# Kernel tuning notes

Measured on AMD Instinct MI355X. Metric: run time of the kernel, lower is better.

The kernel has to match this reference:

```python
import jax, jax.numpy as jnp
import numpy as np

CUTOFFS = [0, 10000, 20000, 40000, 50000]  # cutoff_ends incl. 0 and n_token
D_PROJ = 1024
D_EMBED = 1024
DIV_VAL = 4
N_TOKENS = 4096  # len*bsz flattened


def setup_inputs() -> dict:
    key = jax.random.key(0)
    ks = jax.random.split(key, 12)
    scale = 0.02
    sizes = [CUTOFFS[i + 1] - CUTOFFS[i] for i in range(4)]
    dims = [D_EMBED // DIV_VAL ** i for i in range(4)]  # 1024, 256, 64, 16
    inp = {
        "hidden": jax.random.normal(ks[0], (N_TOKENS, D_PROJ), jnp.float32),
        "target": jax.random.randint(ks[1], (N_TOKENS,), 0, CUTOFFS[-1]),
    }
    for i in range(4):
        inp[f"w{i}"] = jax.random.normal(ks[2 + i], (sizes[i], dims[i]), jnp.float32) * scale
        inp[f"b{i}"] = jnp.zeros((sizes[i],), jnp.float32)  # bias_scale=0.0 -> zeros
        inp[f"p{i}"] = jax.random.normal(ks[6 + i], (D_PROJ, dims[i]), jnp.float32) * scale
    inp["cluster_weight"] = jax.random.normal(ks[10], (3, D_EMBED), jnp.float32) * scale
    inp["cluster_bias"] = jnp.zeros((3,), jnp.float32)
    return inp


def reference(hidden, target, w0, b0, p0, w1, b1, p1, w2, b2, p2, w3, b3, p3,
              cluster_weight, cluster_bias):
    # head = shortlist weights + cluster logits rows  -> [10003, d_embed]
    head_w = jnp.concatenate([w0, cluster_weight], axis=0)
    head_b = jnp.concatenate([b0, cluster_bias], axis=0)
    head_logit = (hidden @ p0) @ head_w.T + head_b          # [N, 10003]
    head_lp = jax.nn.log_softmax(head_logit, axis=-1)
    rows = jnp.arange(hidden.shape[0])
    head_size = head_w.shape[0]

    # cluster 0 (shortlist): gather head log-prob at target
    mask0 = target < CUTOFFS[1]
    lp = jnp.where(mask0, head_lp[rows, jnp.clip(target, 0, CUTOFFS[1] - 1)], 0.0)

    # tail clusters i=1..3: head_logprob[:, -i] + tail log-prob at (target - l_idx)
    for i, (w, b, p) in enumerate([(w1, b1, p1), (w2, b2, p2), (w3, b3, p3)], start=1):
        l, r = CUTOFFS[i], CUTOFFS[i + 1]
        mask = (target >= l) & (target < r)
        tail_lp = jax.nn.log_softmax((hidden @ p) @ w.T + b, axis=-1)  # [N, r-l]
        g = tail_lp[rows, jnp.clip(target - l, 0, r - l - 1)]
        lp = lp + jnp.where(mask, head_lp[:, head_size - i] + g, 0.0)

    return -lp.mean()
```

## Files before the change

kernel.cpp:

```cpp
#include <hip/hip_runtime.h>
#include <hip/hip_fp8.h>
#include <math.h>

typedef __bf16 bf16;
typedef __attribute__((ext_vector_type(8))) __bf16 bf16x8;
typedef __attribute__((ext_vector_type(4))) float f32x4;
typedef __attribute__((ext_vector_type(16))) float f32x16;
typedef __attribute__((ext_vector_type(8))) int i32x8;

#define M_TOK 4096
#define MREF 8.0f


__device__ __forceinline__ void gl_lds16(const void* g, void* l) {
  __builtin_amdgcn_global_load_lds(
      (const __attribute__((address_space(1))) unsigned int*)g,
      (__attribute__((address_space(3))) unsigned int*)l, 16, 0, 0);
}

__device__ __forceinline__ int xcd_swz(int idx, int nwg) {
  int xcd = idx & 7, pos = idx >> 3;
  int q = nwg >> 3, r = nwg & 7;
  int base = xcd < r ? xcd * (q + 1) : r * (q + 1) + (xcd - r) * q;
  return base + pos;
}

__device__ __forceinline__ unsigned char f2fp8(float v) {
  __hip_fp8_e4m3 h(v);
  return (unsigned char)h.__x;
}
__device__ __forceinline__ float fp82f(unsigned char b) {
  __hip_fp8_e4m3 h;
  h.__x = (__hip_fp8_storage_t)b;
  return (float)h;
}

struct bf16x4s { bf16 a, b, c, d; };


#define NB0 4096
#define NB1 10240
#define NB2 2528
#define NB3 1256
#define NB4 316
#define NB5 352
#define NB6 198

__global__ __launch_bounds__(256) void prep(
    const float* __restrict__ hidden, const float* __restrict__ w0,
    const float* __restrict__ cw, const float* __restrict__ w1,
    const float* __restrict__ w2, const float* __restrict__ w3,
    const float* __restrict__ p0, const float* __restrict__ p1,
    const float* __restrict__ p2, const float* __restrict__ p3,
    const float* __restrict__ b0, const float* __restrict__ cb,
    const float* __restrict__ b1, const float* __restrict__ b2,
    const float* __restrict__ b3, const int* __restrict__ target,
    unsigned char* __restrict__ hiddenF8, unsigned char* __restrict__ headwF8,
    bf16* __restrict__ w1p, bf16* __restrict__ w2p, bf16* __restrict__ w3p,
    unsigned char* __restrict__ pF8,
    float* __restrict__ headb, float* __restrict__ t1b,
    float* __restrict__ t2b, float* __restrict__ t3b,
    int* __restrict__ r1, int* __restrict__ r2, int* __restrict__ r3,
    int* __restrict__ posmap, int* __restrict__ counts) {
  __shared__ float tile[64][65];
  __shared__ unsigned long long sd[256];
  int b = blockIdx.x, t = threadIdx.x;
  if (b < NB0) {
    long i = (long)b * 256 + t;
    float4 v = ((const float4*)hidden)[i];
    unsigned int u = (unsigned int)f2fp8(v.x) | ((unsigned int)f2fp8(v.y) << 8) |
                     ((unsigned int)f2fp8(v.z) << 16) | ((unsigned int)f2fp8(v.w) << 24);
    ((unsigned int*)hiddenF8)[i] = u;
    return;
  }
  b -= NB0;
  if (b < NB1) {
    long i = (long)b * 256 + t;
    int row = (int)(i >> 8), c4 = ((int)i & 255) * 4;
    float4 v;
    if (row < 10000)      v = *(const float4*)(w0 + (long)row * 1024 + c4);
    else if (row < 10003) v = *(const float4*)(cw + (long)(row - 10000) * 1024 + c4);
    else                  v = make_float4(0.f, 0.f, 0.f, 0.f);
    unsigned int u = (unsigned int)f2fp8(v.x) | ((unsigned int)f2fp8(v.y) << 8) |
                     ((unsigned int)f2fp8(v.z) << 16) | ((unsigned int)f2fp8(v.w) << 24);
    ((unsigned int*)headwF8)[i] = u;
    return;
  }
  b -= NB1;
  if (b < NB2) {
    long i = (long)b * 256 + t;
    int row = (int)(i >> 6), c4 = ((int)i & 63) * 4;
    float4 v = row < 10000 ? *(const float4*)(w1 + (long)row * 256 + c4)
                           : make_float4(0.f, 0.f, 0.f, 0.f);
    bf16x4s o; o.a = (bf16)v.x; o.b = (bf16)v.y; o.c = (bf16)v.z; o.d = (bf16)v.w;
    ((bf16x4s*)w1p)[i] = o;
    return;
  }
  b -= NB2;
  if (b < NB3) {
    long i = (long)b * 256 + t;
    int row = (int)(i >> 4), c4 = ((int)i & 15) * 4;
    float4 v = row < 20000 ? *(const float4*)(w2 + (long)row * 64 + c4)
                           : make_float4(0.f, 0.f, 0.f, 0.f);
    bf16x4s o; o.a = (bf16)v.x; o.b = (bf16)v.y; o.c = (bf16)v.z; o.d = (bf16)v.w;
    ((bf16x4s*)w2p)[i] = o;
    return;
  }
  b -= NB3;
  if (b < NB4) {
    long i = (long)b * 256 + t;
    int row = (int)(i >> 3), c4 = ((int)i & 7) * 4;
    float4 v = (row < 10000 && c4 < 16) ? *(const float4*)(w3 + (long)row * 16 + c4)
                                        : make_float4(0.f, 0.f, 0.f, 0.f);
    bf16x4s o; o.a = (bf16)v.x; o.b = (bf16)v.y; o.c = (bf16)v.z; o.d = (bf16)v.w;
    ((bf16x4s*)w3p)[i] = o;
    return;
  }
  b -= NB4;
  if (b < NB5) {
    int tk = b & 15, tn = b >> 4;
    int kb = tk * 64, nb = tn * 64;
    const float* src; int N, segn;
    if (tn < 16)      { src = p0; N = 1024; segn = nb; }
    else if (tn < 20) { src = p1; N = 256;  segn = nb - 1024; }
    else if (tn < 21) { src = p2; N = 64;   segn = 0; }
    else              { src = p3; N = 16;   segn = 0; }
    int tx = t & 63, ty = t >> 6;
#pragma unroll
    for (int kk = ty; kk < 64; kk += 4)
      tile[kk][tx] = (segn + tx < N) ? src[(long)(kb + kk) * N + segn + tx] : 0.f;
    __syncthreads();
#pragma unroll
    for (int nn = ty; nn < 64; nn += 4)
      pF8[(long)(nb + nn) * 1024 + kb + tx] = f2fp8(tile[tx][nn]);
    return;
  }
  b -= NB5;
  if (b < NB6) {
    int i = b * 256 + t;
    if (i < 10240) {
      headb[i] = i < 10000 ? b0[i] : (i < 10003 ? cb[i - 10000] : -3.0e38f);
    } else if (i < 10240 + 10112) {
      int j = i - 10240; t1b[j] = j < 10000 ? b1[j] : -3.0e38f;
    } else if (i < 10240 + 10112 + 20096) {
      int j = i - 10240 - 10112; t2b[j] = j < 20000 ? b2[j] : -3.0e38f;
    } else if (i < 10240 + 10112 + 20096 + 10112) {
      int j = i - 10240 - 10112 - 20096; t3b[j] = j < 10000 ? b3[j] : -3.0e38f;
    }
    return;
  }
  {
    int c1 = 0, c2 = 0, c3 = 0;
#pragma unroll
    for (int j = 0; j < 16; ++j) {
      int tt = target[t * 16 + j];
      if (tt >= 10000) { if (tt < 20000) ++c1; else if (tt < 40000) ++c2; else ++c3; }
    }
    unsigned long long packed = (unsigned long long)c1 |
                                ((unsigned long long)c2 << 21) |
                                ((unsigned long long)c3 << 42);
    sd[t] = packed;
    __syncthreads();
    for (int off = 1; off < 256; off <<= 1) {
      unsigned long long add = t >= off ? sd[t - off] : 0ULL;
      __syncthreads();
      sd[t] += add;
      __syncthreads();
    }
    unsigned long long excl = sd[t] - packed;
    const unsigned long long M21 = (1ULL << 21) - 1;
    int p1i = (int)(excl & M21), p2i = (int)((excl >> 21) & M21), p3i = (int)(excl >> 42);
#pragma unroll
    for (int j = 0; j < 16; ++j) {
      int row = t * 16 + j;
      int tt = target[row];
      if (tt >= 10000) {
        if (tt < 20000)      { r1[p1i] = row; posmap[row] = p1i; ++p1i; }
        else if (tt < 40000) { r2[p2i] = row; posmap[row] = p2i; ++p2i; }
        else                 { r3[p3i] = row; posmap[row] = p3i; ++p3i; }
      }
    }
    if (t == 255) {
      unsigned long long tot = sd[255];
      counts[1] = (int)(tot & M21);
      counts[2] = (int)((tot >> 21) & M21);
      counts[3] = (int)(tot >> 42);
    }
  }
}


template<int MODE>
__global__ __launch_bounds__(256, 2) void f8gemm(
    const unsigned char* __restrict__ A,
    const unsigned char* __restrict__ B,
    unsigned char* __restrict__ Cf8, bf16* __restrict__ Cbf,
    const float* __restrict__ bias,
    float* __restrict__ Ps, int nslot) {
  int bid = blockIdx.x;
  int xcd = bid & 7, pos = bid >> 3;
  int tile = pos >> 2;
  int rowblk = (xcd << 2) | (pos & 3);
  int rowbase = rowblk * 128;
  int tid = threadIdx.x;
  int w = tid >> 6, l = tid & 63;
  int l31 = l & 31, lh = l >> 5;
  int wr = w >> 1, wc = w & 1;

  __shared__ __align__(16) unsigned char As[2][128 * 128];
  __shared__ __align__(16) unsigned char Bs[2][128 * 128];

  int srow = tid >> 3;
  int slot = tid & 7;
  const unsigned char* ga[4];
  const unsigned char* gb[4];
#pragma unroll
  for (int c = 0; c < 4; ++c) {
    int lrow = c * 32 + srow;
    int gslot = slot ^ ((lrow ^ (lrow >> 3)) & 7);
    ga[c] = A + (long)(rowbase + lrow) * 1024 + gslot * 16;
    gb[c] = B + (long)(tile * 128 + lrow) * 1024 + gslot * 16;
  }

  f32x16 acc[2][2];
#pragma unroll
  for (int m = 0; m < 2; ++m)
#pragma unroll
    for (int n = 0; n < 2; ++n)
#pragma unroll
      for (int g = 0; g < 16; ++g) acc[m][n][g] = 0.f;

#pragma unroll
  for (int c = 0; c < 4; ++c) {
    gl_lds16(ga[c], &As[0][c * 4096 + tid * 16]);
    gl_lds16(gb[c], &Bs[0][c * 4096 + tid * 16]);
  }

  int cur = 0;
#pragma unroll
  for (int i = 0; i < 8; ++i) {
    if (i < 7) {
      int nxt = cur ^ 1;
      int k0 = (i + 1) * 128;
#pragma unroll
      for (int c = 0; c < 4; ++c) {
        gl_lds16(ga[c] + k0, &As[nxt][c * 4096 + tid * 16]);
        gl_lds16(gb[c] + k0, &Bs[nxt][c * 4096 + tid * 16]);
      }
      asm volatile("s_waitcnt vmcnt(8)" ::: "memory");
    } else {
      asm volatile("s_waitcnt vmcnt(0)" ::: "memory");
    }
    __builtin_amdgcn_s_barrier();
    __builtin_amdgcn_sched_barrier(0);

    const unsigned char* Ab = &As[cur][0];
    const unsigned char* Bb = &Bs[cur][0];
#pragma unroll
    for (int kk = 0; kk < 2; ++kk) {
      i32x8 af[2], bfr[2];
#pragma unroll
      for (int m = 0; m < 2; ++m) {
        int ar = wr * 64 + m * 32 + l31;
        int f = (ar ^ (ar >> 3)) & 7;
        int s0 = (kk * 4 + lh * 2) ^ f;
        int s1 = (kk * 4 + lh * 2 + 1) ^ f;
        int4 lo = *(const int4*)(Ab + ar * 128 + s0 * 16);
        int4 hi = *(const int4*)(Ab + ar * 128 + s1 * 16);
        af[m][0] = lo.x; af[m][1] = lo.y; af[m][2] = lo.z; af[m][3] = lo.w;
        af[m][4] = hi.x; af[m][5] = hi.y; af[m][6] = hi.z; af[m][7] = hi.w;
      }
#pragma unroll
      for (int n = 0; n < 2; ++n) {
        int br = wc * 64 + n * 32 + l31;
        int f = (br ^ (br >> 3)) & 7;
        int s0 = (kk * 4 + lh * 2) ^ f;
        int s1 = (kk * 4 + lh * 2 + 1) ^ f;
        int4 lo = *(const int4*)(Bb + br * 128 + s0 * 16);
        int4 hi = *(const int4*)(Bb + br * 128 + s1 * 16);
        bfr[n][0] = lo.x; bfr[n][1] = lo.y; bfr[n][2] = lo.z; bfr[n][3] = lo.w;
        bfr[n][4] = hi.x; bfr[n][5] = hi.y; bfr[n][6] = hi.z; bfr[n][7] = hi.w;
      }
#pragma unroll
      for (int m = 0; m < 2; ++m)
#pragma unroll
        for (int n = 0; n < 2; ++n)
          acc[m][n] = __builtin_amdgcn_mfma_scale_f32_32x32x64_f8f6f4(
              af[m], bfr[n], acc[m][n], 0, 0, 0, 0x7F7F7F7F, 0, 0x7F7F7F7F);
    }
    __builtin_amdgcn_s_barrier();
    cur ^= 1;
  }
  __builtin_amdgcn_sched_barrier(0);

  if (MODE == 0) {
    unsigned char* Ls = &As[0][0];
    int col0 = tile * 128;
    if (col0 < 1024) {
#pragma unroll
      for (int m = 0; m < 2; ++m)
#pragma unroll
        for (int n = 0; n < 2; ++n) {
          int col = wc * 64 + n * 32 + l31;
#pragma unroll
          for (int g = 0; g < 16; ++g) {
            int row = wr * 64 + m * 32 + (g & 3) + 8 * (g >> 2) + 4 * lh;
            Ls[row * 128 + col] = f2fp8(acc[m][n][g]);
          }
        }
      __syncthreads();
      int row = tid >> 1, half = tid & 1;
      unsigned char* gp = Cf8 + (long)(rowbase + row) * 1024 + col0 + half * 64;
#pragma unroll
      for (int j = 0; j < 4; ++j)
        *(int4*)(gp + j * 16) = *(const int4*)(Ls + tid * 64 + j * 16);
    } else {
      bf16* Lb = (bf16*)Ls;
#pragma unroll
      for (int m = 0; m < 2; ++m)
#pragma unroll
        for (int n = 0; n < 2; ++n) {
          int col = wc * 64 + n * 32 + l31;
#pragma unroll
          for (int g = 0; g < 16; ++g) {
            int row = wr * 64 + m * 32 + (g & 3) + 8 * (g >> 2) + 4 * lh;
            Lb[row * 128 + col] = (bf16)acc[m][n][g];
          }
        }
      __syncthreads();
      int row = tid >> 1, half = tid & 1;
      bf16* gp = Cbf + (long)(rowbase + row) * 384 + (col0 - 1024) + half * 64;
#pragma unroll
      for (int j = 0; j < 8; ++j)
        *(int4*)(gp + j * 8) = *(const int4*)(Ls + tid * 128 + j * 16);
    }
  } else {
    float rs[2][16];
#pragma unroll
    for (int m = 0; m < 2; ++m)
#pragma unroll
      for (int g = 0; g < 16; ++g) rs[m][g] = 0.f;
    int col0 = tile * 128;
#pragma unroll
    for (int n = 0; n < 2; ++n) {
      float bv = bias[col0 + wc * 64 + n * 32 + l31];
#pragma unroll
      for (int m = 0; m < 2; ++m)
#pragma unroll
        for (int g = 0; g < 16; ++g)
          rs[m][g] += __expf(acc[m][n][g] + bv - MREF);
    }
#pragma unroll
    for (int m = 0; m < 2; ++m)
#pragma unroll
      for (int g = 0; g < 16; ++g) {
        float v = rs[m][g];
        v += __shfl_xor(v, 1);
        v += __shfl_xor(v, 2);
        v += __shfl_xor(v, 4);
        v += __shfl_xor(v, 8);
        v += __shfl_xor(v, 16);
        rs[m][g] = v;
      }
    if (l31 == 0) {
      int slotP = tile * 2 + wc;
#pragma unroll
      for (int m = 0; m < 2; ++m)
#pragma unroll
        for (int g = 0; g < 16; ++g) {
          int row = rowbase + wr * 64 + m * 32 + (g & 3) + 8 * (g >> 2) + 4 * lh;
          Ps[(long)row * nslot + slotP] = rs[m][g];
        }
    }
  }
}


template<int K>
__global__ __launch_bounds__(256, 3) void tail_lse(
    const bf16* __restrict__ A, int lda,
    const bf16* __restrict__ B, int nTiles, int tpb,
    const float* __restrict__ bias,
    float* __restrict__ Ps, int nslot,
    const int* __restrict__ rowidx, const int* __restrict__ counts, int cluster) {
  int wg = xcd_swz(blockIdx.x, gridDim.x);
  int split = wg >> 5;
  int rowblk = wg & 31;
  int rowbase = rowblk * 128;
  int nc = counts[cluster];
  if (rowbase >= nc) return;
  int tid = threadIdx.x;
  int w = tid >> 6, llo = tid & 15, lhi = (tid >> 4) & 3;
  int wr = w >> 1, wc = w & 1;

  __shared__ __align__(16) bf16 As[128 * 32];
  __shared__ __align__(16) bf16 Bs[128 * 32];

  int srow = tid >> 2;
  int selem = (tid & 3) * 8;
  int sr0 = rowbase + srow, sr1 = sr0 + 64;
  sr0 = rowidx[sr0 < nc ? sr0 : nc - 1];
  sr1 = rowidx[sr1 < nc ? sr1 : nc - 1];
  const bf16* ga0 = A + (long)sr0 * lda + selem;
  const bf16* ga1 = A + (long)sr1 * lda + selem;
  bf16* la0 = As + tid * 8;
  bf16* la1 = As + 2048 + tid * 8;
  bf16* lb0 = Bs + tid * 8;
  bf16* lb1 = Bs + 2048 + tid * 8;

  float rs[4][4];
#pragma unroll
  for (int a = 0; a < 4; ++a)
#pragma unroll
    for (int bq = 0; bq < 4; ++bq) rs[a][bq] = 0.f;

  int t0 = split * tpb;
  int tE = t0 + tpb; if (tE > nTiles) tE = nTiles;

  for (int tile = t0; tile < tE; ++tile) {
    int col0 = tile * 128;
    const bf16* gb0 = B + (long)(col0 + srow) * K + selem;
    const bf16* gb1 = gb0 + (long)64 * K;

    f32x4 acc[4][4];
    f32x4 zero = {0.f, 0.f, 0.f, 0.f};
#pragma unroll
    for (int a = 0; a < 4; ++a)
#pragma unroll
      for (int bq = 0; bq < 4; ++bq) acc[a][bq] = zero;

    for (int k0 = 0; k0 < K; k0 += 32) {
      gl_lds16(ga0 + k0, la0);
      gl_lds16(ga1 + k0, la1);
      gl_lds16(gb0 + k0, lb0);
      gl_lds16(gb1 + k0, lb1);
      __syncthreads();
      bf16x8 af[4], bf_[4];
#pragma unroll
      for (int m = 0; m < 4; ++m)
        af[m] = *(const bf16x8*)(As + (wr * 64 + m * 16 + llo) * 32 + lhi * 8);
#pragma unroll
      for (int n = 0; n < 4; ++n)
        bf_[n] = *(const bf16x8*)(Bs + (wc * 64 + n * 16 + llo) * 32 + lhi * 8);
#pragma unroll
      for (int m = 0; m < 4; ++m)
#pragma unroll
        for (int n = 0; n < 4; ++n)
          acc[m][n] = __builtin_amdgcn_mfma_f32_16x16x32_bf16(af[m], bf_[n], acc[m][n], 0, 0, 0);
      __syncthreads();
    }

    float bv[4];
#pragma unroll
    for (int n = 0; n < 4; ++n) bv[n] = bias[col0 + wc * 64 + n * 16 + llo];
#pragma unroll
    for (int mm = 0; mm < 4; ++mm)
#pragma unroll
      for (int r = 0; r < 4; ++r)
#pragma unroll
        for (int n = 0; n < 4; ++n)
          rs[mm][r] += __expf(acc[mm][n][r] + bv[n] - MREF);
  }

#pragma unroll
  for (int mm = 0; mm < 4; ++mm) {
#pragma unroll
    for (int r = 0; r < 4; ++r) {
      float vv = rs[mm][r];
      vv += __shfl_xor(vv, 1);
      vv += __shfl_xor(vv, 2);
      vv += __shfl_xor(vv, 4);
      vv += __shfl_xor(vv, 8);
      if (llo == 0) {
        int crow = rowbase + wr * 64 + mm * 16 + lhi * 4 + r;
        Ps[(long)crow * nslot + (split * 2 + wc)] = vv;
      }
    }
  }
}


__global__ __launch_bounds__(256) void merge_lp(
    const int* __restrict__ target, const int* __restrict__ posmap,
    const unsigned char* __restrict__ projF8, const unsigned char* __restrict__ headw,
    const float* __restrict__ headb, const bf16* __restrict__ projT,
    const bf16* __restrict__ w1p, const float* __restrict__ t1b,
    const bf16* __restrict__ w2p, const float* __restrict__ t2b,
    const bf16* __restrict__ w3p, const float* __restrict__ t3b,
    const float* __restrict__ hs, int NSH,
    const float* __restrict__ s1, int NS1,
    const float* __restrict__ s2, int NS2,
    const float* __restrict__ s3, int NS3,
    float* __restrict__ lp) {
  int lane = threadIdx.x & 63;
  int row = (blockIdx.x * 256 + threadIdx.x) >> 6;
  if (row >= M_TOK) return;

  float sh = 0.f;
  for (int sp = lane; sp < NSH; sp += 64) sh += hs[(long)row * NSH + sp];
#pragma unroll
  for (int off = 1; off < 64; off <<= 1) sh += __shfl_xor(sh, off);
  float lseh = MREF + __logf(sh);

  float a[16];
  const unsigned char* ap = projF8 + (long)row * 1024 + lane * 16;
#pragma unroll
  for (int j = 0; j < 16; ++j) a[j] = fp82f(ap[j]);
  int t = target[row];
  int c0 = t < 10000 ? t : 9999;
  float hd[4];
#pragma unroll
  for (int q = 0; q < 4; ++q) {
    int col = q == 0 ? c0 : 9999 + q;
    const unsigned char* wp = headw + (long)col * 1024 + lane * 16;
    float d = 0.f;
#pragma unroll
    for (int j = 0; j < 16; ++j) d += a[j] * fp82f(wp[j]);
#pragma unroll
    for (int off = 1; off < 64; off <<= 1) d += __shfl_xor(d, off);
    hd[q] = d + headb[col];
  }

  float res;
  if (t < 10000) {
    res = hd[0] - lseh;
  } else {
    const float* sP; const bf16* wP; const float* bP;
    int NS, q, Kt, offT, base;
    if (t < 20000)      { sP = s1; wP = w1p; bP = t1b; NS = NS1; q = 3; Kt = 256; offT = 0;   base = 10000; }
    else if (t < 40000) { sP = s2; wP = w2p; bP = t2b; NS = NS2; q = 2; Kt = 64;  offT = 256; base = 20000; }
    else                { sP = s3; wP = w3p; bP = t3b; NS = NS3; q = 1; Kt = 32;  offT = 320; base = 40000; }
    int pos = posmap[row];
    float ss = 0.f;
    for (int sp = lane; sp < NS; sp += 64) ss += sP[(long)pos * NS + sp];
#pragma unroll
    for (int off = 1; off < 64; off <<= 1) ss += __shfl_xor(ss, off);
    float lset = MREF + __logf(ss);
    int wrow = t - base;
    float gt = 0.f;
    for (int k = lane; k < Kt; k += 64)
      gt += (float)projT[(long)row * 384 + offT + k] * (float)wP[(long)wrow * Kt + k];
#pragma unroll
    for (int off = 1; off < 64; off <<= 1) gt += __shfl_xor(gt, off);
    gt += bP[wrow];
    res = (hd[q] - lseh) + (gt - lset);
  }
  if (lane == 0) lp[row] = res;
}

__global__ void neg_mean(const float* __restrict__ lp, float* __restrict__ out) {
  __shared__ float red[256];
  float s = 0.f;
  for (int i = threadIdx.x; i < M_TOK; i += 256) s += lp[i];
  red[threadIdx.x] = s;
  __syncthreads();
  for (int o = 128; o > 0; o >>= 1) {
    if (threadIdx.x < o) red[threadIdx.x] += red[threadIdx.x + o];
    __syncthreads();
  }
  if (threadIdx.x == 0) out[0] = -red[0] / (float)M_TOK;
}


extern "C" void kernel_launch(void* const* d_in, const int* in_sizes, int n_in,
                              void* d_out, int out_size, void* d_ws, size_t ws_size,
                              hipStream_t stream) {
  const float* hidden = (const float*)d_in[0];
  const int*   target = (const int*)d_in[1];
  const float* w0 = (const float*)d_in[2];
  const float* b0 = (const float*)d_in[3];
  const float* p0 = (const float*)d_in[4];
  const float* w1 = (const float*)d_in[5];
  const float* b1 = (const float*)d_in[6];
  const float* p1 = (const float*)d_in[7];
  const float* w2 = (const float*)d_in[8];
  const float* b2 = (const float*)d_in[9];
  const float* p2 = (const float*)d_in[10];
  const float* w3 = (const float*)d_in[11];
  const float* b3 = (const float*)d_in[12];
  const float* p3 = (const float*)d_in[13];
  const float* cw = (const float*)d_in[14];
  const float* cb = (const float*)d_in[15];

  const int NH = 10240;
  const int N1 = 10112, N2 = 20096, N3 = 10112;
  const int TH = NH / 128;
  const int T1t = 79, T2t = 157, T3t = 79;
  const int TPB_1 = 1, TPB_2 = 2, TPB_3 = 1;
  const int S1 = 79, S2 = 79, S3 = 79;
  const int NSH = TH * 2, NS1 = S1 * 2, NS2 = S2 * 2, NS3 = S3 * 2;

  char* ws = (char*)d_ws;
  size_t off = 0;
  auto alloc = [&](size_t bytes) -> char* {
    char* p = ws + off;
    off += (bytes + 255) & ~(size_t)255;
    return p;
  };
  unsigned char* hiddenF8 = (unsigned char*)alloc(4096L * 1024);
  unsigned char* pF8      = (unsigned char*)alloc(1408L * 1024);
  unsigned char* headwF8  = (unsigned char*)alloc((long)NH * 1024);
  bf16* w1p   = (bf16*)alloc((long)N1 * 256 * 2);
  bf16* w2p   = (bf16*)alloc((long)N2 * 64 * 2);
  bf16* w3p   = (bf16*)alloc((long)N3 * 32 * 2);
  unsigned char* projF8 = (unsigned char*)alloc(4096L * 1024);
  bf16* projT = (bf16*)alloc(4096L * 384 * 2);
  float* headb = (float*)alloc((long)NH * 4);
  float* t1b   = (float*)alloc((long)N1 * 4);
  float* t2b   = (float*)alloc((long)N2 * 4);
  float* t3b   = (float*)alloc((long)N3 * 4);
  float* hsP = (float*)alloc((size_t)M_TOK * NSH * 4);
  float* s1P = (float*)alloc((size_t)M_TOK * NS1 * 4);
  float* s2P = (float*)alloc((size_t)M_TOK * NS2 * 4);
  float* s3P = (float*)alloc((size_t)M_TOK * NS3 * 4);
  float* lp  = (float*)alloc((size_t)M_TOK * 4);
  int* r1 = (int*)alloc((size_t)M_TOK * 4);
  int* r2 = (int*)alloc((size_t)M_TOK * 4);
  int* r3 = (int*)alloc((size_t)M_TOK * 4);
  int* posmap = (int*)alloc((size_t)M_TOK * 4);
  int* counts = (int*)alloc(16);
  if (ws_size < off) return;

  const int PREP_BLOCKS = NB0 + NB1 + NB2 + NB3 + NB4 + NB5 + NB6 + 1;
  prep<<<PREP_BLOCKS, 256, 0, stream>>>(
      hidden, w0, cw, w1, w2, w3, p0, p1, p2, p3, b0, cb, b1, b2, b3, target,
      hiddenF8, headwF8, w1p, w2p, w3p, pF8, headb, t1b, t2b, t3b,
      r1, r2, r3, posmap, counts);

  f8gemm<0><<<11 * 32, 256, 0, stream>>>(
      hiddenF8, pF8, projF8, projT, nullptr, nullptr, 0);

  f8gemm<1><<<TH * 32, 256, 0, stream>>>(
      projF8, headwF8, nullptr, nullptr, headb, hsP, NSH);

  tail_lse<256><<<S1 * 32, 256, 0, stream>>>(
      projT, 384, w1p, T1t, TPB_1, t1b, s1P, NS1, r1, counts, 1);
  tail_lse<64><<<S2 * 32, 256, 0, stream>>>(
      projT + 256, 384, w2p, T2t, TPB_2, t2b, s2P, NS2, r2, counts, 2);
  tail_lse<32><<<S3 * 32, 256, 0, stream>>>(
      projT + 320, 384, w3p, T3t, TPB_3, t3b, s3P, NS3, r3, counts, 3);

  merge_lp<<<1024, 256, 0, stream>>>(
      target, posmap, projF8, headwF8, headb, projT,
      w1p, t1b, w2p, t2b, w3p, t3b,
      hsP, NSH, s1P, NS1, s2P, NS2, s3P, NS3, lp);

  neg_mean<<<1, 256, 0, stream>>>(lp, (float*)d_out);
}
```

Measured before the change: 154.2 us.

## Halve FP8 GEMM K-tile to 64 to cut LDS and raise occupancy

The FP8 GEMM's K-step drops from 128 to 64 bytes per stage, so the double-buffered LDS footprint shrinks from 64KB to 32KB. Launch bounds go from 2 to 4 blocks per CU, and the swizzle becomes a 4-slot XOR pattern to match. The main loop now runs 16 iterations with one MFMA step each instead of 8 with two. Higher occupancy should hide memory latency better, at the cost of twice as many barriers and waitcnt syncs, and the tighter register budget may cause spills.

```diff
diff --git a/kernel.cpp b/kernel.cpp
--- a/kernel.cpp
+++ b/kernel.cpp
@@ -191,7 +191,7 @@
 
 
 template<int MODE>
-__global__ __launch_bounds__(256, 2) void f8gemm(
+__global__ __launch_bounds__(256, 4) void f8gemm(
     const unsigned char* __restrict__ A,
     const unsigned char* __restrict__ B,
     unsigned char* __restrict__ Cf8, bf16* __restrict__ Cbf,
@@ -207,17 +207,16 @@
   int l31 = l & 31, lh = l >> 5;
   int wr = w >> 1, wc = w & 1;
 
-  __shared__ __align__(16) unsigned char As[2][128 * 128];
-  __shared__ __align__(16) unsigned char Bs[2][128 * 128];
-
-  int srow = tid >> 3;
-  int slot = tid & 7;
-  const unsigned char* ga[4];
-  const unsigned char* gb[4];
-#pragma unroll
-  for (int c = 0; c < 4; ++c) {
-    int lrow = c * 32 + srow;
-    int gslot = slot ^ ((lrow ^ (lrow >> 3)) & 7);
+  __shared__ __align__(16) unsigned char SMEM[32768];
+
+  int srow = tid >> 2;
+  int slot = tid & 3;
+  const unsigned char* ga[2];
+  const unsigned char* gb[2];
+#pragma unroll
+  for (int c = 0; c < 2; ++c) {
+    int lrow = c * 64 + srow;
+    int gslot = slot ^ ((lrow ^ (lrow >> 2)) & 3);
     ga[c] = A + (long)(rowbase + lrow) * 1024 + gslot * 16;
     gb[c] = B + (long)(tile * 128 + lrow) * 1024 + gslot * 16;
   }
@@ -231,70 +230,66 @@
       for (int g = 0; g < 16; ++g) acc[m][n][g] = 0.f;
 
 #pragma unroll
-  for (int c = 0; c < 4; ++c) {
-    gl_lds16(ga[c], &As[0][c * 4096 + tid * 16]);
-    gl_lds16(gb[c], &Bs[0][c * 4096 + tid * 16]);
+  for (int c = 0; c < 2; ++c) {
+    gl_lds16(ga[c], SMEM + c * 4096 + tid * 16);
+    gl_lds16(gb[c], SMEM + 16384 + c * 4096 + tid * 16);
   }
 
   int cur = 0;
 #pragma unroll
-  for (int i = 0; i < 8; ++i) {
-    if (i < 7) {
+  for (int i = 0; i < 16; ++i) {
+    if (i < 15) {
       int nxt = cur ^ 1;
-      int k0 = (i + 1) * 128;
-#pragma unroll
-      for (int c = 0; c < 4; ++c) {
-        gl_lds16(ga[c] + k0, &As[nxt][c * 4096 + tid * 16]);
-        gl_lds16(gb[c] + k0, &Bs[nxt][c * 4096 + tid * 16]);
+      int k0 = (i + 1) * 64;
+#pragma unroll
+      for (int c = 0; c < 2; ++c) {
+        gl_lds16(ga[c] + k0, SMEM + nxt * 8192 + c * 4096 + tid * 16);
+        gl_lds16(gb[c] + k0, SMEM + 16384 + nxt * 8192 + c * 4096 + tid * 16);
       }
-      asm volatile("s_waitcnt vmcnt(8)" ::: "memory");
+      asm volatile("s_waitcnt vmcnt(4)" ::: "memory");
     } else {
       asm volatile("s_waitcnt vmcnt(0)" ::: "memory");
     }
     __builtin_amdgcn_s_barrier();
     __builtin_amdgcn_sched_barrier(0);
 
-    const unsigned char* Ab = &As[cur][0];
-    const unsigned char* Bb = &Bs[cur][0];
-#pragma unroll
-    for (int kk = 0; kk < 2; ++kk) {
-      i32x8 af[2], bfr[2];
-#pragma unroll
-      for (int m = 0; m < 2; ++m) {
-        int ar = wr * 64 + m * 32 + l31;
-        int f = (ar ^ (ar >> 3)) & 7;
-        int s0 = (kk * 4 + lh * 2) ^ f;
-        int s1 = (kk * 4 + lh * 2 + 1) ^ f;
-        int4 lo = *(const int4*)(Ab + ar * 128 + s0 * 16);
-        int4 hi = *(const int4*)(Ab + ar * 128 + s1 * 16);
-        af[m][0] = lo.x; af[m][1] = lo.y; af[m][2] = lo.z; af[m][3] = lo.w;
-        af[m][4] = hi.x; af[m][5] = hi.y; af[m][6] = hi.z; af[m][7] = hi.w;
-      }
-#pragma unroll
-      for (int n = 0; n < 2; ++n) {
-        int br = wc * 64 + n * 32 + l31;
-        int f = (br ^ (br >> 3)) & 7;
-        int s0 = (kk * 4 + lh * 2) ^ f;
-        int s1 = (kk * 4 + lh * 2 + 1) ^ f;
-        int4 lo = *(const int4*)(Bb + br * 128 + s0 * 16);
-        int4 hi = *(const int4*)(Bb + br * 128 + s1 * 16);
-        bfr[n][0] = lo.x; bfr[n][1] = lo.y; bfr[n][2] = lo.z; bfr[n][3] = lo.w;
-        bfr[n][4] = hi.x; bfr[n][5] = hi.y; bfr[n][6] = hi.z; bfr[n][7] = hi.w;
-      }
-#pragma unroll
-      for (int m = 0; m < 2; ++m)
-#pragma unroll
-        for (int n = 0; n < 2; ++n)
-          acc[m][n] = __builtin_amdgcn_mfma_scale_f32_32x32x64_f8f6f4(
-              af[m], bfr[n], acc[m][n], 0, 0, 0, 0x7F7F7F7F, 0, 0x7F7F7F7F);
-    }
+    const unsigned char* Ab = SMEM + cur * 8192;
+    const unsigned char* Bb = SMEM + 16384 + cur * 8192;
+    i32x8 af[2], bfr[2];
+#pragma unroll
+    for (int m = 0; m < 2; ++m) {
+      int ar = wr * 64 + m * 32 + l31;
+      int f = (ar ^ (ar >> 2)) & 3;
+      int s0 = (lh * 2) ^ f;
+      int s1 = (lh * 2 + 1) ^ f;
+      int4 lo = *(const int4*)(Ab + ar * 64 + s0 * 16);
+      int4 hi = *(const int4*)(Ab + ar * 64 + s1 * 16);
+      af[m][0] = lo.x; af[m][1] = lo.y; af[m][2] = lo.z; af[m][3] = lo.w;
+      af[m][4] = hi.x; af[m][5] = hi.y; af[m][6] = hi.z; af[m][7] = hi.w;
+    }
+#pragma unroll
+    for (int n = 0; n < 2; ++n) {
+      int br = wc * 64 + n * 32 + l31;
+      int f = (br ^ (br >> 2)) & 3;
+      int s0 = (lh * 2) ^ f;
+      int s1 = (lh * 2 + 1) ^ f;
+      int4 lo = *(const int4*)(Bb + br * 64 + s0 * 16);
+      int4 hi = *(const int4*)(Bb + br * 64 + s1 * 16);
+      bfr[n][0] = lo.x; bfr[n][1] = lo.y; bfr[n][2] = lo.z; bfr[n][3] = lo.w;
+      bfr[n][4] = hi.x; bfr[n][5] = hi.y; bfr[n][6] = hi.z; bfr[n][7] = hi.w;
+    }
+#pragma unroll
+    for (int m = 0; m < 2; ++m)
+#pragma unroll
+      for (int n = 0; n < 2; ++n)
+        acc[m][n] = __builtin_amdgcn_mfma_scale_f32_32x32x64_f8f6f4(
+            af[m], bfr[n], acc[m][n], 0, 0, 0, 0x7F7F7F7F, 0, 0x7F7F7F7F);
     __builtin_amdgcn_s_barrier();
     cur ^= 1;
   }
   __builtin_amdgcn_sched_barrier(0);
 
   if (MODE == 0) {
-    unsigned char* Ls = &As[0][0];
     int col0 = tile * 128;
     if (col0 < 1024) {
 #pragma unroll
@@ -305,7 +300,7 @@
 #pragma unroll
           for (int g = 0; g < 16; ++g) {
             int row = wr * 64 + m * 32 + (g & 3) + 8 * (g >> 2) + 4 * lh;
-            Ls[row * 128 + col] = f2fp8(acc[m][n][g]);
+            SMEM[row * 128 + col] = f2fp8(acc[m][n][g]);
           }
         }
       __syncthreads();
@@ -313,9 +308,9 @@
       unsigned char* gp = Cf8 + (long)(rowbase + row) * 1024 + col0 + half * 64;
 #pragma unroll
       for (int j = 0; j < 4; ++j)
-        *(int4*)(gp + j * 16) = *(const int4*)(Ls + tid * 64 + j * 16);
+        *(int4*)(gp + j * 16) = *(const int4*)(SMEM + tid * 64 + j * 16);
     } else {
-      bf16* Lb = (bf16*)Ls;
+      bf16* Lb = (bf16*)SMEM;
 #pragma unroll
       for (int m = 0; m < 2; ++m)
 #pragma unroll
@@ -332,7 +327,7 @@
       bf16* gp = Cbf + (long)(rowbase + row) * 384 + (col0 - 1024) + half * 64;
 #pragma unroll
       for (int j = 0; j < 8; ++j)
-        *(int4*)(gp + j * 8) = *(const int4*)(Ls + tid * 128 + j * 16);
+        *(int4*)(gp + j * 8) = *(const int4*)(SMEM + tid * 128 + j * 16);
     }
   } else {
     float rs[2][16];
```

After: 150.4 us, median of 2. 2.5% less time.
